# Kernel optimization log

Hardware: AMD Instinct MI355X
Metric: run time of the kernel (lower is better)

The kernel has to match this reference:

```python
import jax, jax.numpy as jnp
import numpy as np

D = 1024      # input_dim / hidden_size
H = 16        # n_heads
HD = D // H   # head_size = 64
F = 4096      # mlp_dim
EPS = 1e-6


def setup_inputs() -> dict:
    key = jax.random.key(0)
    ks = jax.random.split(key, 16)
    s = 0.02
    inp = {
        "x": jax.random.normal(ks[0], (4, 2048, D), dtype=jnp.float32),
        # attention params (torch Linear: y = x @ W.T + b; we store W as [out,in])
        "Wq": jax.random.normal(ks[1], (D, D), dtype=jnp.float32) * s,
        "bq": jax.random.normal(ks[2], (D,), dtype=jnp.float32) * s,
        "Wk": jax.random.normal(ks[3], (D, D), dtype=jnp.float32) * s,
        "bk": jax.random.normal(ks[4], (D,), dtype=jnp.float32) * s,
        "Wv": jax.random.normal(ks[5], (D, D), dtype=jnp.float32) * s,
        "bv": jax.random.normal(ks[6], (D,), dtype=jnp.float32) * s,
        "Wo": jax.random.normal(ks[7], (D, D), dtype=jnp.float32) * s,
        "bo": jax.random.normal(ks[8], (D,), dtype=jnp.float32) * s,
        # MLP params
        "W1": jax.random.normal(ks[9], (F, D), dtype=jnp.float32) * s,
        "b1": jax.random.normal(ks[10], (F,), dtype=jnp.float32) * s,
        "W2": jax.random.normal(ks[11], (D, F), dtype=jnp.float32) * s,
        "b2": jax.random.normal(ks[12], (D,), dtype=jnp.float32) * s,
        # LayerNorm params
        "ln1_g": jnp.ones((D,), dtype=jnp.float32),
        "ln1_b": jnp.zeros((D,), dtype=jnp.float32),
        "ln2_g": jnp.ones((D,), dtype=jnp.float32),
        "ln2_b": jnp.zeros((D,), dtype=jnp.float32),
    }
    return inp


def _layernorm(x, g, b):
    mu = jnp.mean(x, axis=-1, keepdims=True)
    var = jnp.mean(jnp.square(x - mu), axis=-1, keepdims=True)
    return (x - mu) * jax.lax.rsqrt(var + EPS) * g + b


def reference(x, Wq, bq, Wk, bk, Wv, bv, Wo, bo, W1, b1, W2, b2,
              ln1_g, ln1_b, ln2_g, ln2_b):
    B, S, _ = x.shape
    h = x
    xn = _layernorm(x, ln1_g, ln1_b)
    # Q/K/V projections -> [B, H, S, HD]
    def split_heads(t):
        return t.reshape(B, S, H, HD).transpose(0, 2, 1, 3)
    q = split_heads(xn @ Wq.T + bq)
    k = split_heads(xn @ Wk.T + bk)
    v = split_heads(xn @ Wv.T + bv)
    scores = jnp.einsum('bhqd,bhkd->bhqk', q, k) / np.sqrt(HD).astype(np.float32)
    probs = jax.nn.softmax(scores, axis=-1)
    ctx = jnp.einsum('bhqk,bhkd->bhqd', probs, v)      # [B,H,S,HD]
    ctx = ctx.transpose(0, 2, 1, 3).reshape(B, S, D)
    attn_out = ctx @ Wo.T + bo
    x = attn_out + h
    h = x
    xn = _layernorm(x, ln2_g, ln2_b)
    y = jax.nn.gelu(xn @ W1.T + b1, approximate=False)  # torch nn.GELU() = exact erf gelu
    y = y @ W2.T + b2
    return y + h
```

## Files before the change

### kernel.cpp

```cpp
#include <hip/hip_runtime.h>
#include <hip/hip_bf16.h>
#include <math.h>

typedef __attribute__((ext_vector_type(8))) short short8;
typedef __attribute__((ext_vector_type(4))) float f32x4;

#define MFMA_BF16 __builtin_amdgcn_mfma_f32_16x16x32_bf16

__device__ __forceinline__ ushort f2bf(float f) {
  union { __hip_bfloat16 h; ushort u; } c;
  c.h = __float2bfloat16(f);
  return c.u;
}
__device__ __forceinline__ void async_cp16(const ushort* g, ushort* l) {
  __builtin_amdgcn_global_load_lds(
      (const __attribute__((address_space(1))) void*)g,
      (__attribute__((address_space(3))) void*)l, 16, 0, 0);
}

__global__ __launch_bounds__(256) void conv_all(
    const float* __restrict__ Wq, const float* __restrict__ Wk,
    const float* __restrict__ Wv, const float* __restrict__ Wo,
    const float* __restrict__ W1, const float* __restrict__ W2,
    const float* __restrict__ bq, const float* __restrict__ bk,
    const float* __restrict__ bv,
    ushort* __restrict__ wqkv, ushort* __restrict__ wo,
    ushort* __restrict__ w1, ushort* __restrict__ w2,
    float* __restrict__ bqkv) {
  int i = blockIdx.x * 256 + threadIdx.x;
  if (i < 3145728) {
    const float* src; ushort* dst; int off;
    if (i < 786432)        {
      dst = wqkv; off = i;
      if (i < 262144)      src = Wq + (size_t)i * 4;
      else if (i < 524288) src = Wk + (size_t)(i - 262144) * 4;
      else                 src = Wv + (size_t)(i - 524288) * 4;
    } else if (i < 1048576) { dst = wo; off = i - 786432;  src = Wo + (size_t)off * 4; }
    else if (i < 2097152)   { dst = w1; off = i - 1048576; src = W1 + (size_t)off * 4; }
    else                    { dst = w2; off = i - 2097152; src = W2 + (size_t)off * 4; }
    float4 v = *(const float4*)src;
    ushort4 o;
    o.x = f2bf(v.x); o.y = f2bf(v.y); o.z = f2bf(v.z); o.w = f2bf(v.w);
    ((ushort4*)dst)[off] = o;
  } else if (i < 3146496) {
    int off = i - 3145728;
    const float* src;
    if (off < 256)      src = bq + (size_t)off * 4;
    else if (off < 512) src = bk + (size_t)(off - 256) * 4;
    else                src = bv + (size_t)(off - 512) * 4;
    ((float4*)bqkv)[off] = *(const float4*)src;
  }
}

__global__ __launch_bounds__(256) void ln_kernel(const float* __restrict__ x,
    const float* __restrict__ g, const float* __restrict__ b,
    ushort* __restrict__ out) {
  const int row = blockIdx.x, t = threadIdx.x;
  float4 v = ((const float4*)(x + (size_t)row * 1024))[t];
  float s  = v.x + v.y + v.z + v.w;
  float ss = v.x*v.x + v.y*v.y + v.z*v.z + v.w*v.w;
  #pragma unroll
  for (int off = 32; off >= 1; off >>= 1) {
    s  += __shfl_xor(s, off);
    ss += __shfl_xor(ss, off);
  }
  __shared__ float red[8];
  int wv = t >> 6, ln = t & 63;
  if (ln == 0) { red[wv] = s; red[4 + wv] = ss; }
  __syncthreads();
  float S  = red[0] + red[1] + red[2] + red[3];
  float SS = red[4] + red[5] + red[6] + red[7];
  float mu  = S * (1.0f/1024.0f);
  float var = SS * (1.0f/1024.0f) - mu*mu;
  float rs  = rsqrtf(var + 1e-6f);
  float4 gv = ((const float4*)g)[t];
  float4 bv = ((const float4*)b)[t];
  ushort4 o;
  o.x = f2bf((v.x-mu)*rs*gv.x + bv.x);
  o.y = f2bf((v.y-mu)*rs*gv.y + bv.y);
  o.z = f2bf((v.z-mu)*rs*gv.z + bv.z);
  o.w = f2bf((v.w-mu)*rs*gv.w + bv.w);
  ((ushort4*)(out + (size_t)row*1024))[t] = o;
}

enum { EPI_QK = 0, EPI_VT = 1, EPI_WO = 2, EPI_GELU = 3, EPI_OUT = 4 };

template <int EPI>
__global__ __launch_bounds__(256) void gemm_kernel(const ushort* __restrict__ A,
    const ushort* __restrict__ Bw, const float* __restrict__ bias,
    const float* __restrict__ res, void* __restrict__ outp,
    void* __restrict__ outp2, int K, int N, float scale) {
  __shared__ ushort As[2][128 * 32];
  __shared__ ushort Bs[2][128 * 32];
  const int t = threadIdx.x;
  const int m0 = blockIdx.x * 128, n0 = blockIdx.y * 128;
  const int lane = t & 63, wave = t >> 6;
  const int col = lane & 15, quad = lane >> 4;
  const int wrow = (wave >> 1) * 64, wcol = (wave & 1) * 64;

  f32x4 acc[4][4];
  #pragma unroll
  for (int i = 0; i < 4; i++)
    #pragma unroll
    for (int j = 0; j < 4; j++)
      acc[i][j] = (f32x4){0.f, 0.f, 0.f, 0.f};

  const int lrow = lane >> 2, lcol = (lane & 3) * 8;
  const ushort* Ag = A  + (size_t)(m0 + wave * 32 + lrow) * K + lcol;
  const ushort* Bg = Bw + (size_t)(n0 + wave * 32 + lrow) * K + lcol;
  const int ldso = (wave * 32) * 32;

  for (int k0 = 0; k0 < K; k0 += 64) {
    __syncthreads();
    #pragma unroll
    for (int c = 0; c < 2; c++) {
      async_cp16(Ag + k0 + c * 32,                  &As[c][ldso]);
      async_cp16(Ag + (size_t)16 * K + k0 + c * 32, &As[c][ldso + 16 * 32]);
      async_cp16(Bg + k0 + c * 32,                  &Bs[c][ldso]);
      async_cp16(Bg + (size_t)16 * K + k0 + c * 32, &Bs[c][ldso + 16 * 32]);
    }
    __syncthreads();
    #pragma unroll
    for (int c = 0; c < 2; c++) {
      short8 af[4], bf[4];
      #pragma unroll
      for (int tm = 0; tm < 4; tm++)
        af[tm] = *(const short8*)&As[c][(wrow + tm * 16 + col) * 32 + quad * 8];
      #pragma unroll
      for (int tn = 0; tn < 4; tn++)
        bf[tn] = *(const short8*)&Bs[c][(wcol + tn * 16 + col) * 32 + quad * 8];
      #pragma unroll
      for (int tm = 0; tm < 4; tm++)
        #pragma unroll
        for (int tn = 0; tn < 4; tn++)
          acc[tm][tn] = MFMA_BF16(af[tm], bf[tn], acc[tm][tn], 0, 0, 0);
    }
  }

  #pragma unroll
  for (int tm = 0; tm < 4; tm++) {
    #pragma unroll
    for (int tn = 0; tn < 4; tn++) {
      const int n = n0 + wcol + tn * 16 + col;
      const float bn = (EPI == EPI_VT) ? 0.f : bias[n];
      #pragma unroll
      for (int r = 0; r < 4; r++) {
        const int m = m0 + wrow + tm * 16 + quad * 4 + r;
        float v = acc[tm][tn][r] + bn;
        if (EPI == EPI_VT) {
          float vv = v + bias[m];
          int h = m >> 6, hd = m & 63, bb = n >> 11, s2 = n & 2047;
          ((ushort*)outp)[((size_t)((bb * 16 + h) * 64 + hd)) * 2048 + s2] = f2bf(vv);
        } else if (EPI == EPI_GELU) {
          float u = v * 0.7978845608028654f * (1.0f + 0.044715f * v * v);
          float e = __builtin_amdgcn_exp2f(u * 2.885390081777927f);
          float th = 1.0f - 2.0f * __builtin_amdgcn_rcpf(e + 1.0f);
          ((ushort*)outp)[(size_t)m * N + n] = f2bf(0.5f * v * (1.0f + th));
        } else {
          ((float*)outp)[(size_t)m * N + n] = v + res[(size_t)m * N + n];
        }
      }
    }
  }
}

template <int EPI>
__global__ __launch_bounds__(512, 2) void gemm256_kernel(const ushort* __restrict__ A,
    const ushort* __restrict__ Bw, const float* __restrict__ bias,
    void* __restrict__ outp, void* __restrict__ outp2, int K, int N, float scale) {
  __shared__ ushort As[2][256 * 64];
  __shared__ ushort Bs[2][256 * 64];
  const int t = threadIdx.x;
  const int lane = t & 63, wave = t >> 6;
  const int col = lane & 15, quad = lane >> 4;
  const int m0 = blockIdx.x * 256, n0 = blockIdx.y * 256;
  const int wm = wave >> 2, wn = wave & 3;

  f32x4 acc[8][4];
  #pragma unroll
  for (int i = 0; i < 8; i++)
    #pragma unroll
    for (int j = 0; j < 4; j++)
      acc[i][j] = (f32x4){0.f, 0.f, 0.f, 0.f};

  size_t aoff[4], boff[4];
  int sdst[4];
  #pragma unroll
  for (int i = 0; i < 4; i++) {
    int c = i * 512 + t;
    int row = c >> 3, p = c & 7;
    int gcol = (p ^ (row & 7)) * 8;
    aoff[i] = (size_t)(m0 + row) * K + gcol;
    boff[i] = (size_t)(n0 + row) * K + gcol;
    sdst[i] = c * 8;
  }

  const int NT = K >> 6;
  #pragma unroll
  for (int i = 0; i < 4; i++) {
    async_cp16(A  + aoff[i], &As[0][sdst[i]]);
    async_cp16(Bw + boff[i], &Bs[0][sdst[i]]);
  }

  int cur = 0;
  for (int kt = 0; kt < NT; kt++) {
    if (kt + 1 < NT) {
      const int nxt = cur ^ 1;
      const int ko = (kt + 1) << 6;
      #pragma unroll
      for (int i = 0; i < 4; i++) {
        async_cp16(A  + aoff[i] + ko, &As[nxt][sdst[i]]);
        async_cp16(Bw + boff[i] + ko, &Bs[nxt][sdst[i]]);
      }
      asm volatile("s_waitcnt vmcnt(8)" ::: "memory");
    } else {
      asm volatile("s_waitcnt vmcnt(0)" ::: "memory");
    }
    __builtin_amdgcn_sched_barrier(0);
    __builtin_amdgcn_s_barrier();
    __builtin_amdgcn_sched_barrier(0);

    #pragma unroll
    for (int c = 0; c < 2; c++) {
      short8 af[8], bf[4];
      #pragma unroll
      for (int tm = 0; tm < 8; tm++) {
        const int row = wm * 128 + tm * 16 + col;
        af[tm] = *(const short8*)&As[cur][row * 64 + ((c * 4 + quad) ^ (row & 7)) * 8];
      }
      #pragma unroll
      for (int tn = 0; tn < 4; tn++) {
        const int row = wn * 64 + tn * 16 + col;
        bf[tn] = *(const short8*)&Bs[cur][row * 64 + ((c * 4 + quad) ^ (row & 7)) * 8];
      }
      __builtin_amdgcn_s_setprio(1);
      #pragma unroll
      for (int tm = 0; tm < 8; tm++)
        #pragma unroll
        for (int tn = 0; tn < 4; tn++)
          acc[tm][tn] = MFMA_BF16(af[tm], bf[tn], acc[tm][tn], 0, 0, 0);
      __builtin_amdgcn_s_setprio(0);
    }

    asm volatile("s_waitcnt lgkmcnt(0)" ::: "memory");
    __builtin_amdgcn_sched_barrier(0);
    __builtin_amdgcn_s_barrier();
    cur ^= 1;
  }

  #pragma unroll
  for (int tm = 0; tm < 8; tm++) {
    #pragma unroll
    for (int tn = 0; tn < 4; tn++) {
      const int n = n0 + wn * 64 + tn * 16 + col;
      const float bn = bias[n];
      #pragma unroll
      for (int r = 0; r < 4; r++) {
        const int m = m0 + wm * 128 + tm * 16 + quad * 4 + r;
        float v = acc[tm][tn][r] + bn;
        if (EPI == EPI_QK) {
          int nl = n & 1023, h = nl >> 6, hd = nl & 63;
          int bb = m >> 11, s2 = m & 2047;
          if (n < 1024)
            ((ushort*)outp)[(((size_t)(bb * 16 + h) * 2048 + s2) * 64) + hd] = f2bf(v * scale);
          else
            ((ushort*)outp2)[(((size_t)(bb * 16 + h) * 2048 + s2) * 64) + hd] = f2bf(v);
        } else {
          float u = v * 0.7978845608028654f * (1.0f + 0.044715f * v * v);
          float e = __builtin_amdgcn_exp2f(u * 2.885390081777927f);
          float th = 1.0f - 2.0f * __builtin_amdgcn_rcpf(e + 1.0f);
          ((ushort*)outp)[(size_t)m * N + n] = f2bf(0.5f * v * (1.0f + th));
        }
      }
    }
  }
}

__global__ __launch_bounds__(256) void attn_kernel(const ushort* __restrict__ Qb,
    const ushort* __restrict__ Kb, const ushort* __restrict__ Vt,
    ushort* __restrict__ ctx) {
  const int lane = threadIdx.x & 63, wave = threadIdx.x >> 6;
  const int col = lane & 15, quad = lane >> 4;
  const int bx = blockIdx.x;
  const int bh = bx & 63;
  const int qt = bx >> 6;
  const int qbase = qt * 128 + wave * 32;
  const ushort* Qh = Qb + (size_t)bh * 2048 * 64;
  const ushort* Kh = Kb + (size_t)bh * 2048 * 64;
  const ushort* Vh = Vt + (size_t)bh * 64 * 2048;

  short8 qa[2][2];
  #pragma unroll
  for (int qg = 0; qg < 2; qg++) {
    const ushort* Qr = Qh + (size_t)(qbase + qg * 16 + col) * 64 + quad * 8;
    qa[qg][0] = *(const short8*)Qr;
    qa[qg][1] = *(const short8*)(Qr + 32);
  }

  f32x4 Ot[2][4];
  float l_part[2];
  #pragma unroll
  for (int qg = 0; qg < 2; qg++) {
    l_part[qg] = 0.f;
    #pragma unroll
    for (int dt = 0; dt < 4; dt++) Ot[qg][dt] = (f32x4){0.f, 0.f, 0.f, 0.f};
  }

  __shared__ ushort Ks[2][2][64 * 32];
  __shared__ ushort Vs[2][2][64 * 32];
  __shared__ ushort P_lds[4][16][64];

  const int lrow = lane >> 2;
  const int srow = wave * 16 + lrow;
  const int lcol = ((lane & 3) ^ ((srow >> 1) & 3)) * 8;
  const ushort* Kg = Kh + (size_t)srow * 64 + lcol;
  const ushort* Vg = Vh + (size_t)srow * 2048 + lcol;
  const int so = (wave * 16) * 32;

  const int kvswz = (col >> 1) & 3;
  const int pswz = col & 7;

  async_cp16(Kg,      &Ks[0][0][so]);
  async_cp16(Kg + 32, &Ks[0][1][so]);
  async_cp16(Vg,      &Vs[0][0][so]);
  async_cp16(Vg + 32, &Vs[0][1][so]);
  __syncthreads();

  int cur = 0;
  for (int kb = 0; kb < 2048; kb += 64) {
    if (kb + 64 < 2048) {
      const int nxt = cur ^ 1;
      async_cp16(Kg + (size_t)(kb + 64) * 64,      &Ks[nxt][0][so]);
      async_cp16(Kg + (size_t)(kb + 64) * 64 + 32, &Ks[nxt][1][so]);
      async_cp16(Vg + (kb + 64),                   &Vs[nxt][0][so]);
      async_cp16(Vg + (kb + 64) + 32,              &Vs[nxt][1][so]);
    }

    short8 kf[4][2], vf[4][2];
    #pragma unroll
    for (int kt = 0; kt < 4; kt++)
      #pragma unroll
      for (int c = 0; c < 2; c++)
        kf[kt][c] = *(const short8*)&Ks[cur][c][(kt * 16 + col) * 32 + (quad ^ kvswz) * 8];
    #pragma unroll
    for (int dt = 0; dt < 4; dt++)
      #pragma unroll
      for (int c = 0; c < 2; c++)
        vf[dt][c] = *(const short8*)&Vs[cur][c][(dt * 16 + col) * 32 + (quad ^ kvswz) * 8];

    #pragma unroll
    for (int qg = 0; qg < 2; qg++) {
      f32x4 s[4];
      __builtin_amdgcn_s_setprio(1);
      #pragma unroll
      for (int kt = 0; kt < 4; kt++) {
        s[kt] = (f32x4){0.f, 0.f, 0.f, 0.f};
        s[kt] = MFMA_BF16(kf[kt][0], qa[qg][0], s[kt], 0, 0, 0);
        s[kt] = MFMA_BF16(kf[kt][1], qa[qg][1], s[kt], 0, 0, 0);
      }
      __builtin_amdgcn_s_setprio(0);
      ushort(*P)[64] = P_lds[wave];
      #pragma unroll
      for (int kt = 0; kt < 4; kt++) {
        float p0 = __builtin_amdgcn_exp2f(s[kt][0]);
        float p1 = __builtin_amdgcn_exp2f(s[kt][1]);
        float p2 = __builtin_amdgcn_exp2f(s[kt][2]);
        float p3 = __builtin_amdgcn_exp2f(s[kt][3]);
        l_part[qg] += (p0 + p1) + (p2 + p3);
        uint2 pk;
        asm("v_cvt_pk_bf16_f32 %0, %1, %2" : "=v"(pk.x) : "v"(p0), "v"(p1));
        asm("v_cvt_pk_bf16_f32 %0, %1, %2" : "=v"(pk.y) : "v"(p2), "v"(p3));
        *(uint2*)&P[col][(((2 * kt + (quad >> 1)) ^ pswz) * 8) + (quad & 1) * 4] = pk;
      }
      #pragma unroll
      for (int c = 0; c < 2; c++) {
        short8 pf = *(const short8*)&P_lds[wave][col][((4 * c + quad) ^ pswz) * 8];
        __builtin_amdgcn_s_setprio(1);
        #pragma unroll
        for (int dt = 0; dt < 4; dt++)
          Ot[qg][dt] = MFMA_BF16(vf[dt][c], pf, Ot[qg][dt], 0, 0, 0);
        __builtin_amdgcn_s_setprio(0);
      }
    }
    __syncthreads();
    cur ^= 1;
  }

  const int bb = bh >> 4, h = bh & 15;
  #pragma unroll
  for (int qg = 0; qg < 2; qg++) {
    float l = l_part[qg];
    l += __shfl_xor(l, 16);
    l += __shfl_xor(l, 32);
    float inv = __builtin_amdgcn_rcpf(l);
    const int q = qbase + qg * 16 + col;
    size_t base = ((size_t)(bb * 2048 + q)) * 1024 + h * 64;
    #pragma unroll
    for (int dt = 0; dt < 4; dt++) {
      ushort4 o;
      o.x = f2bf(Ot[qg][dt][0] * inv);
      o.y = f2bf(Ot[qg][dt][1] * inv);
      o.z = f2bf(Ot[qg][dt][2] * inv);
      o.w = f2bf(Ot[qg][dt][3] * inv);
      *(ushort4*)&ctx[base + dt * 16 + quad * 4] = o;
    }
  }
}

extern "C" void kernel_launch(void* const* d_in, const int* in_sizes, int n_in,
                              void* d_out, int out_size, void* d_ws, size_t ws_size,
                              hipStream_t stream) {
  const float* x     = (const float*)d_in[0];
  const float* Wq    = (const float*)d_in[1];
  const float* bq    = (const float*)d_in[2];
  const float* Wk    = (const float*)d_in[3];
  const float* bk    = (const float*)d_in[4];
  const float* Wv    = (const float*)d_in[5];
  const float* bv    = (const float*)d_in[6];
  const float* Wo    = (const float*)d_in[7];
  const float* bo    = (const float*)d_in[8];
  const float* W1    = (const float*)d_in[9];
  const float* b1    = (const float*)d_in[10];
  const float* W2    = (const float*)d_in[11];
  const float* b2    = (const float*)d_in[12];
  const float* ln1_g = (const float*)d_in[13];
  const float* ln1_b = (const float*)d_in[14];
  const float* ln2_g = (const float*)d_in[15];
  const float* ln2_b = (const float*)d_in[16];

  const size_t MB = 1ull << 20;
  char* ws = (char*)d_ws;
  ushort* Wqkv_b = (ushort*)(ws + 0 * MB);
  ushort* Wo_b   = (ushort*)(ws + 6 * MB);
  ushort* W1_b   = (ushort*)(ws + 8 * MB);
  ushort* W2_b   = (ushort*)(ws + 16 * MB);
  ushort* xn1    = (ushort*)(ws + 24 * MB);
  ushort* Qb     = (ushort*)(ws + 40 * MB);
  ushort* Kb     = (ushort*)(ws + 56 * MB);
  ushort* Vt     = (ushort*)(ws + 72 * MB);
  ushort* ctxb   = (ushort*)(ws + 88 * MB);
  float*  x2     = (float*)(ws + 104 * MB);
  ushort* xn2    = (ushort*)(ws + 136 * MB);
  ushort* y1     = (ushort*)(ws + 152 * MB);
  float*  bqkv   = (float*)(ws + 152 * MB);

  conv_all<<<12291, 256, 0, stream>>>(Wq, Wk, Wv, Wo, W1, W2, bq, bk, bv,
                                      Wqkv_b, Wo_b, W1_b, W2_b, bqkv);

  ln_kernel<<<8192, 256, 0, stream>>>(x, ln1_g, ln1_b, xn1);

  const float cs = 0.125f * 1.4426950408889634f;
  gemm256_kernel<EPI_QK><<<dim3(32, 8), 512, 0, stream>>>(
      xn1, Wqkv_b, bqkv, Qb, Kb, 1024, 2048, cs);
  gemm_kernel<EPI_VT><<<dim3(8, 64), 256, 0, stream>>>(
      Wqkv_b + (size_t)2048 * 1024, xn1, bqkv + 2048, nullptr, Vt, nullptr,
      1024, 8192, 1.0f);

  attn_kernel<<<1024, 256, 0, stream>>>(Qb, Kb, Vt, ctxb);

  gemm_kernel<EPI_WO><<<dim3(64, 8), 256, 0, stream>>>(
      ctxb, Wo_b, bo, x, x2, nullptr, 1024, 1024, 1.0f);

  ln_kernel<<<8192, 256, 0, stream>>>(x2, ln2_g, ln2_b, xn2);

  gemm256_kernel<EPI_GELU><<<dim3(32, 16), 512, 0, stream>>>(
      xn2, W1_b, b1, y1, nullptr, 1024, 4096, 1.0f);
  gemm_kernel<EPI_OUT><<<dim3(64, 8), 256, 0, stream>>>(
      y1, W2_b, b2, x2, d_out, nullptr, 4096, 1024, 1.0f);
}
```

Baseline: 521.5 us.

## Load V fragments directly from global into registers, drop V LDS staging

The attention kernel no longer stages V tiles through shared memory. Each lane now loads its V MFMA fragments straight from global memory into registers, double-buffered via ping-pong register arrays, and the loop is unrolled by two so the buffers swap statically. This removes the V LDS writes and reads and halves LDS use, in exchange for more VGPRs and per-wave redundant global reads of V (every wave loads the full V tile), which rely on cache hits.

```diff
diff --git a/kernel.cpp b/kernel.cpp
--- a/kernel.cpp
+++ b/kernel.cpp
@@ -276,6 +276,69 @@
   }
 }
 
+__device__ __forceinline__ void attn_body(
+    int kb, int cur, int prefK, int prefV,
+    const ushort* __restrict__ Kg, const ushort* __restrict__ Vgl,
+    int so, int col, int quad, int wave, int kvswz, int pswz,
+    short8 (&qa)[2][2], short8 (&vc)[4][2], short8 (&vn)[4][2],
+    f32x4 (&Ot)[2][4], float (&l_part)[2],
+    ushort (*Ks)[2][64 * 32], ushort (*P_lds)[16][64]) {
+  if (prefK) {
+    async_cp16(Kg + (size_t)(kb + 64) * 64,      &Ks[cur ^ 1][0][so]);
+    async_cp16(Kg + (size_t)(kb + 64) * 64 + 32, &Ks[cur ^ 1][1][so]);
+  }
+  if (prefV) {
+    #pragma unroll
+    for (int dt = 0; dt < 4; dt++)
+      #pragma unroll
+      for (int c = 0; c < 2; c++)
+        vn[dt][c] = *(const short8*)(Vgl + (size_t)(dt * 16) * 2048 + (kb + 64) + c * 32);
+  }
+
+  short8 kf[4][2];
+  #pragma unroll
+  for (int kt = 0; kt < 4; kt++)
+    #pragma unroll
+    for (int c = 0; c < 2; c++)
+      kf[kt][c] = *(const short8*)&Ks[cur][c][(kt * 16 + col) * 32 + (quad ^ kvswz) * 8];
+
+  #pragma unroll
+  for (int qg = 0; qg < 2; qg++) {
+    f32x4 s[4];
+    __builtin_amdgcn_s_setprio(1);
+    #pragma unroll
+    for (int kt = 0; kt < 4; kt++) {
+      s[kt] = (f32x4){0.f, 0.f, 0.f, 0.f};
+      s[kt] = MFMA_BF16(kf[kt][0], qa[qg][0], s[kt], 0, 0, 0);
+      s[kt] = MFMA_BF16(kf[kt][1], qa[qg][1], s[kt], 0, 0, 0);
+    }
+    __builtin_amdgcn_s_setprio(0);
+    ushort(*P)[64] = P_lds[wave];
+    #pragma unroll
+    for (int kt = 0; kt < 4; kt++) {
+      float p0 = __builtin_amdgcn_exp2f(s[kt][0]);
+      float p1 = __builtin_amdgcn_exp2f(s[kt][1]);
+      float p2 = __builtin_amdgcn_exp2f(s[kt][2]);
+      float p3 = __builtin_amdgcn_exp2f(s[kt][3]);
+      l_part[qg] += (p0 + p1) + (p2 + p3);
+      uint2 pk;
+      asm("v_cvt_pk_bf16_f32 %0, %1, %2" : "=v"(pk.x) : "v"(p0), "v"(p1));
+      asm("v_cvt_pk_bf16_f32 %0, %1, %2" : "=v"(pk.y) : "v"(p2), "v"(p3));
+      *(uint2*)&P[col][(((2 * kt + (quad >> 1)) ^ pswz) * 8) + (quad & 1) * 4] = pk;
+    }
+    #pragma unroll
+    for (int c = 0; c < 2; c++) {
+      short8 pf = *(const short8*)&P_lds[wave][col][((4 * c + quad) ^ pswz) * 8];
+      __builtin_amdgcn_s_setprio(1);
+      #pragma unroll
+      for (int dt = 0; dt < 4; dt++)
+        Ot[qg][dt] = MFMA_BF16(vc[dt][c], pf, Ot[qg][dt], 0, 0, 0);
+      __builtin_amdgcn_s_setprio(0);
+    }
+  }
+  __syncthreads();
+}
+
 __global__ __launch_bounds__(256) void attn_kernel(const ushort* __restrict__ Qb,
     const ushort* __restrict__ Kb, const ushort* __restrict__ Vt,
     ushort* __restrict__ ctx) {
@@ -307,83 +370,36 @@
   }
 
   __shared__ ushort Ks[2][2][64 * 32];
-  __shared__ ushort Vs[2][2][64 * 32];
   __shared__ ushort P_lds[4][16][64];
 
   const int lrow = lane >> 2;
   const int srow = wave * 16 + lrow;
   const int lcol = ((lane & 3) ^ ((srow >> 1) & 3)) * 8;
   const ushort* Kg = Kh + (size_t)srow * 64 + lcol;
-  const ushort* Vg = Vh + (size_t)srow * 2048 + lcol;
   const int so = (wave * 16) * 32;
 
   const int kvswz = (col >> 1) & 3;
   const int pswz = col & 7;
 
+  const ushort* Vgl = Vh + (size_t)col * 2048 + quad * 8;
+
+  short8 vA[4][2], vB[4][2];
+
   async_cp16(Kg,      &Ks[0][0][so]);
   async_cp16(Kg + 32, &Ks[0][1][so]);
-  async_cp16(Vg,      &Vs[0][0][so]);
-  async_cp16(Vg + 32, &Vs[0][1][so]);
+  #pragma unroll
+  for (int dt = 0; dt < 4; dt++)
+    #pragma unroll
+    for (int c = 0; c < 2; c++)
+      vA[dt][c] = *(const short8*)(Vgl + (size_t)(dt * 16) * 2048 + c * 32);
   __syncthreads();
 
-  int cur = 0;
-  for (int kb = 0; kb < 2048; kb += 64) {
-    if (kb + 64 < 2048) {
-      const int nxt = cur ^ 1;
-      async_cp16(Kg + (size_t)(kb + 64) * 64,      &Ks[nxt][0][so]);
-      async_cp16(Kg + (size_t)(kb + 64) * 64 + 32, &Ks[nxt][1][so]);
-      async_cp16(Vg + (kb + 64),                   &Vs[nxt][0][so]);
-      async_cp16(Vg + (kb + 64) + 32,              &Vs[nxt][1][so]);
-    }
-
-    short8 kf[4][2], vf[4][2];
-    #pragma unroll
-    for (int kt = 0; kt < 4; kt++)
-      #pragma unroll
-      for (int c = 0; c < 2; c++)
-        kf[kt][c] = *(const short8*)&Ks[cur][c][(kt * 16 + col) * 32 + (quad ^ kvswz) * 8];
-    #pragma unroll
-    for (int dt = 0; dt < 4; dt++)
-      #pragma unroll
-      for (int c = 0; c < 2; c++)
-        vf[dt][c] = *(const short8*)&Vs[cur][c][(dt * 16 + col) * 32 + (quad ^ kvswz) * 8];
-
-    #pragma unroll
-    for (int qg = 0; qg < 2; qg++) {
-      f32x4 s[4];
-      __builtin_amdgcn_s_setprio(1);
-      #pragma unroll
-      for (int kt = 0; kt < 4; kt++) {
-        s[kt] = (f32x4){0.f, 0.f, 0.f, 0.f};
-        s[kt] = MFMA_BF16(kf[kt][0], qa[qg][0], s[kt], 0, 0, 0);
-        s[kt] = MFMA_BF16(kf[kt][1], qa[qg][1], s[kt], 0, 0, 0);
-      }
-      __builtin_amdgcn_s_setprio(0);
-      ushort(*P)[64] = P_lds[wave];
-      #pragma unroll
-      for (int kt = 0; kt < 4; kt++) {
-        float p0 = __builtin_amdgcn_exp2f(s[kt][0]);
-        float p1 = __builtin_amdgcn_exp2f(s[kt][1]);
-        float p2 = __builtin_amdgcn_exp2f(s[kt][2]);
-        float p3 = __builtin_amdgcn_exp2f(s[kt][3]);
-        l_part[qg] += (p0 + p1) + (p2 + p3);
-        uint2 pk;
-        asm("v_cvt_pk_bf16_f32 %0, %1, %2" : "=v"(pk.x) : "v"(p0), "v"(p1));
-        asm("v_cvt_pk_bf16_f32 %0, %1, %2" : "=v"(pk.y) : "v"(p2), "v"(p3));
-        *(uint2*)&P[col][(((2 * kt + (quad >> 1)) ^ pswz) * 8) + (quad & 1) * 4] = pk;
-      }
-      #pragma unroll
-      for (int c = 0; c < 2; c++) {
-        short8 pf = *(const short8*)&P_lds[wave][col][((4 * c + quad) ^ pswz) * 8];
-        __builtin_amdgcn_s_setprio(1);
-        #pragma unroll
-        for (int dt = 0; dt < 4; dt++)
-          Ot[qg][dt] = MFMA_BF16(vf[dt][c], pf, Ot[qg][dt], 0, 0, 0);
-        __builtin_amdgcn_s_setprio(0);
-      }
-    }
-    __syncthreads();
-    cur ^= 1;
+  for (int kb = 0; kb < 2048; kb += 128) {
+    const int more = (kb + 128 < 2048);
+    attn_body(kb,      0, 1,    1,    Kg, Vgl, so, col, quad, wave, kvswz, pswz,
+              qa, vA, vB, Ot, l_part, Ks, P_lds);
+    attn_body(kb + 64, 1, more, more, Kg, Vgl, so, col, quad, wave, kvswz, pswz,
+              qa, vB, vA, Ot, l_part, Ks, P_lds);
   }
 
   const int bb = bh >> 4, h = bh & 15;
```

Measured after the change: 559.9 us. 1.07x slower.

## Split 256x256 GEMM k-step into four phased quadrant sub-tiles with staggered prefetch

Applied to the files above, without the earlier changes.

Each k-tile is now split into four phases over 128x128 quadrants of the output. Every phase loads a smaller set of A/B fragments from LDS, issues one quarter of the next tile's async global-to-LDS copies, then runs 16 MFMAs. Waves are also remapped so each one owns interleaved rows and columns across the quadrants. The goal is to overlap LDS reads, global prefetch and MFMA work more finely, in the style of an 8-wave ping-pong schedule, and to lower register pressure for fragments. The cost is more barriers per k-step and tighter waitcnt bookkeeping.

```diff
diff --git a/kernel.cpp b/kernel.cpp
--- a/kernel.cpp
+++ b/kernel.cpp
@@ -183,80 +183,105 @@
     for (int j = 0; j < 4; j++)
       acc[i][j] = (f32x4){0.f, 0.f, 0.f, 0.f};
 
-  size_t aoff[4], boff[4];
-  int sdst[4];
-  #pragma unroll
-  for (int i = 0; i < 4; i++) {
-    int c = i * 512 + t;
-    int row = c >> 3, p = c & 7;
-    int gcol = (p ^ (row & 7)) * 8;
-    aoff[i] = (size_t)(m0 + row) * K + gcol;
-    boff[i] = (size_t)(n0 + row) * K + gcol;
-    sdst[i] = c * 8;
-  }
+  size_t aoff[2], boff[2];
+  int d0[2];
+  #pragma unroll
+  for (int i = 0; i < 2; i++) {
+    int c = i * 512 + t, r = c >> 3, p = c & 7;
+    aoff[i] = (size_t)(m0 + r) * K + (p ^ (r & 7)) * 8;
+    boff[i] = (size_t)(n0 + r) * K + (p ^ (r & 7)) * 8;
+    d0[i] = c * 8;
+  }
+  const size_t up = (size_t)128 * K;
 
   const int NT = K >> 6;
   #pragma unroll
-  for (int i = 0; i < 4; i++) {
-    async_cp16(A  + aoff[i], &As[0][sdst[i]]);
-    async_cp16(Bw + boff[i], &Bs[0][sdst[i]]);
-  }
-
-  int cur = 0;
+  for (int i = 0; i < 2; i++) async_cp16(A  + aoff[i],      &As[0][d0[i]]);
+  #pragma unroll
+  for (int i = 0; i < 2; i++) async_cp16(Bw + boff[i],      &Bs[0][d0[i]]);
+  #pragma unroll
+  for (int i = 0; i < 2; i++) async_cp16(A  + aoff[i] + up, &As[0][8192 + d0[i]]);
+  #pragma unroll
+  for (int i = 0; i < 2; i++) async_cp16(Bw + boff[i] + up, &Bs[0][8192 + d0[i]]);
+  asm volatile("s_waitcnt vmcnt(4)" ::: "memory");
+  __builtin_amdgcn_sched_barrier(0);
+  __builtin_amdgcn_s_barrier();
+  __builtin_amdgcn_sched_barrier(0);
+
+  short8 af[4][2], bf[2][2];
   for (int kt = 0; kt < NT; kt++) {
-    if (kt + 1 < NT) {
-      const int nxt = cur ^ 1;
-      const int ko = (kt + 1) << 6;
-      #pragma unroll
-      for (int i = 0; i < 4; i++) {
-        async_cp16(A  + aoff[i] + ko, &As[nxt][sdst[i]]);
-        async_cp16(Bw + boff[i] + ko, &Bs[nxt][sdst[i]]);
-      }
-      asm volatile("s_waitcnt vmcnt(8)" ::: "memory");
-    } else {
-      asm volatile("s_waitcnt vmcnt(0)" ::: "memory");
-    }
-    __builtin_amdgcn_sched_barrier(0);
-    __builtin_amdgcn_s_barrier();
-    __builtin_amdgcn_sched_barrier(0);
-
-    #pragma unroll
-    for (int c = 0; c < 2; c++) {
-      short8 af[8], bf[4];
-      #pragma unroll
-      for (int tm = 0; tm < 8; tm++) {
-        const int row = wm * 128 + tm * 16 + col;
-        af[tm] = *(const short8*)&As[cur][row * 64 + ((c * 4 + quad) ^ (row & 7)) * 8];
-      }
-      #pragma unroll
-      for (int tn = 0; tn < 4; tn++) {
-        const int row = wn * 64 + tn * 16 + col;
-        bf[tn] = *(const short8*)&Bs[cur][row * 64 + ((c * 4 + quad) ^ (row & 7)) * 8];
-      }
+    const int cur = kt & 1, nxt = cur ^ 1;
+    const size_t ko = (size_t)(kt + 1) << 6;
+    const bool more = (kt + 1 < NT);
+    #pragma unroll
+    for (int ph = 0; ph < 4; ph++) {
+      const int ha = ph & 1;
+      const int hb = ph >> 1;
+      #pragma unroll
+      for (int tml = 0; tml < 4; tml++) {
+        const int row = ha * 128 + wm * 64 + tml * 16 + col;
+        #pragma unroll
+        for (int c = 0; c < 2; c++)
+          af[tml][c] = *(const short8*)&As[cur][row * 64 + (((c * 4 + quad) ^ (row & 7)) * 8)];
+      }
+      if (ph == 0 || ph == 2) {
+        #pragma unroll
+        for (int tnl = 0; tnl < 2; tnl++) {
+          const int row = hb * 128 + wn * 32 + tnl * 16 + col;
+          #pragma unroll
+          for (int c = 0; c < 2; c++)
+            bf[tnl][c] = *(const short8*)&Bs[cur][row * 64 + (((c * 4 + quad) ^ (row & 7)) * 8)];
+        }
+      }
+      if (more) {
+        if (ph == 0) {
+          #pragma unroll
+          for (int i = 0; i < 2; i++) async_cp16(A  + aoff[i] + ko,      &As[nxt][d0[i]]);
+        } else if (ph == 1) {
+          #pragma unroll
+          for (int i = 0; i < 2; i++) async_cp16(Bw + boff[i] + ko,      &Bs[nxt][d0[i]]);
+        } else if (ph == 2) {
+          #pragma unroll
+          for (int i = 0; i < 2; i++) async_cp16(A  + aoff[i] + up + ko, &As[nxt][8192 + d0[i]]);
+        } else {
+          #pragma unroll
+          for (int i = 0; i < 2; i++) async_cp16(Bw + boff[i] + up + ko, &Bs[nxt][8192 + d0[i]]);
+        }
+        asm volatile("s_waitcnt vmcnt(4)" ::: "memory");
+      } else {
+        if (ph == 0)      asm volatile("s_waitcnt vmcnt(2)" ::: "memory");
+        else              asm volatile("s_waitcnt vmcnt(0)" ::: "memory");
+      }
+      __builtin_amdgcn_sched_barrier(0);
+      __builtin_amdgcn_s_barrier();
+      asm volatile("s_waitcnt lgkmcnt(0)" ::: "memory");
+      __builtin_amdgcn_sched_barrier(0);
       __builtin_amdgcn_s_setprio(1);
       #pragma unroll
-      for (int tm = 0; tm < 8; tm++)
+      for (int tml = 0; tml < 4; tml++)
         #pragma unroll
-        for (int tn = 0; tn < 4; tn++)
-          acc[tm][tn] = MFMA_BF16(af[tm], bf[tn], acc[tm][tn], 0, 0, 0);
+        for (int tnl = 0; tnl < 2; tnl++) {
+          acc[ha*4+tml][hb*2+tnl] = MFMA_BF16(af[tml][0], bf[tnl][0], acc[ha*4+tml][hb*2+tnl], 0, 0, 0);
+          acc[ha*4+tml][hb*2+tnl] = MFMA_BF16(af[tml][1], bf[tnl][1], acc[ha*4+tml][hb*2+tnl], 0, 0, 0);
+        }
       __builtin_amdgcn_s_setprio(0);
-    }
-
-    asm volatile("s_waitcnt lgkmcnt(0)" ::: "memory");
-    __builtin_amdgcn_sched_barrier(0);
-    __builtin_amdgcn_s_barrier();
-    cur ^= 1;
+      __builtin_amdgcn_sched_barrier(0);
+      __builtin_amdgcn_s_barrier();
+      __builtin_amdgcn_sched_barrier(0);
+    }
   }
 
   #pragma unroll
   for (int tm = 0; tm < 8; tm++) {
+    const int ha = tm >> 2, tml = tm & 3;
     #pragma unroll
     for (int tn = 0; tn < 4; tn++) {
-      const int n = n0 + wn * 64 + tn * 16 + col;
+      const int hb = tn >> 1, tnl = tn & 1;
+      const int n = n0 + hb * 128 + wn * 32 + tnl * 16 + col;
       const float bn = bias[n];
       #pragma unroll
       for (int r = 0; r < 4; r++) {
-        const int m = m0 + wm * 128 + tm * 16 + quad * 4 + r;
+        const int m = m0 + ha * 128 + wm * 64 + tml * 16 + quad * 4 + r;
         float v = acc[tm][tn][r] + bn;
         if (EPI == EPI_QK) {
           int nl = n & 1023, h = nl >> 6, hd = nl & 63;
```

Result: faster. 510.3 us (-2.2%).
